# Performance work log

Hardware: AMD Instinct MI355X
Metric: run time of the kernel (lower is better)

Reference implementation:

```python
import jax, jax.numpy as jnp
import numpy as np

B, T, D = 512, 128, 512   # batch, encoder positions, input_size
H = 512                   # hidden_size
MID, BOT = 38, 38         # class counts


def setup_inputs() -> dict:
    key = jax.random.key(0)
    ks = jax.random.split(key, 12)
    s = lambda fan_in: 1.0 / np.sqrt(fan_in)
    inp = {
        "batch_H": jax.random.normal(ks[0], (B, T, D), dtype=jnp.float32),
        "mid_prev_text": jax.random.randint(ks[1], (B, 26), 0, MID, dtype=jnp.int64)
            if jax.config.jax_enable_x64 else jax.random.randint(ks[1], (B, 26), 0, MID).astype(jnp.int32),
        "bot_text": jax.random.randint(ks[2], (B, 26), 0, BOT).astype(jnp.int32),
        # AttentionCell params
        "W_i2h": jax.random.uniform(ks[3], (H, D), jnp.float32, -s(D), s(D)),
        "W_h2h": jax.random.uniform(ks[4], (H, H), jnp.float32, -s(H), s(H)),
        "b_h2h": jax.random.uniform(ks[5], (H,), jnp.float32, -s(H), s(H)),
        "W_score": jax.random.uniform(ks[6], (1, H), jnp.float32, -s(H), s(H)),
        # LSTMCell params: input dim = D + MID + BOT
        "W_ih": jax.random.uniform(ks[7], (4 * H, D + MID + BOT), jnp.float32, -s(H), s(H)),
        "W_hh": jax.random.uniform(ks[8], (4 * H, H), jnp.float32, -s(H), s(H)),
        "b_ih": jax.random.uniform(ks[9], (4 * H,), jnp.float32, -s(H), s(H)),
        "b_hh": jax.random.uniform(ks[10], (4 * H,), jnp.float32, -s(H), s(H)),
        # generator
        "W_gen": jax.random.uniform(ks[11], (MID, H), jnp.float32, -s(H), s(H)),
        "b_gen": jnp.zeros((MID,), jnp.float32),
        "batch_max_length": 25,
    }
    return inp


def reference(batch_H, mid_prev_text, bot_text, W_i2h, W_h2h, b_h2h, W_score,
              W_ih, W_hh, b_ih, b_hh, W_gen, b_gen, batch_max_length):
    num_steps = batch_max_length + 1
    bsz = batch_H.shape[0]
    hid = W_h2h.shape[0]

    # batch_H projection is step-independent: compute once. [B, T, H]
    batch_H_proj = jnp.einsum('btd,hd->bth', batch_H, W_i2h)

    # Precompute teacher-forced onehots, time-major: [num_steps, B, C]
    oh_mid = jax.nn.one_hot(mid_prev_text[:, :num_steps].T, MID, dtype=batch_H.dtype)
    oh_bot = jax.nn.one_hot(bot_text[:, :num_steps].T, BOT, dtype=batch_H.dtype)

    def step(carry, inputs):
        h, c = carry
        ohm, ohb = inputs
        # attention scores over T positions
        prev_proj = h @ W_h2h.T + b_h2h                       # [B, H]
        e = jnp.einsum('bth,oh->bto', jnp.tanh(batch_H_proj + prev_proj[:, None, :]), W_score)  # [B,T,1]
        alpha = jax.nn.softmax(e, axis=1)                     # [B, T, 1]
        context = jnp.einsum('bto,btd->bd', alpha, batch_H)   # [B, D]
        x = jnp.concatenate([context, ohm, ohb], axis=1)      # [B, D+MID+BOT]
        # LSTMCell (PyTorch gate order: i, f, g, o)
        gates = x @ W_ih.T + b_ih + h @ W_hh.T + b_hh         # [B, 4H]
        i_g, f_g, g_g, o_g = jnp.split(gates, 4, axis=1)
        i_g = jax.nn.sigmoid(i_g)
        f_g = jax.nn.sigmoid(f_g)
        g_g = jnp.tanh(g_g)
        o_g = jax.nn.sigmoid(o_g)
        c_new = f_g * c + i_g * g_g
        h_new = o_g * jnp.tanh(c_new)
        return (h_new, c_new), h_new

    h0 = jnp.zeros((bsz, hid), batch_H.dtype)
    c0 = jnp.zeros((bsz, hid), batch_H.dtype)
    (_, _), hiddens = jax.lax.scan(step, (h0, c0), (oh_mid, oh_bot))  # [S, B, H]
    output_hiddens = jnp.transpose(hiddens, (1, 0, 2))                 # [B, S, H]
    g = jnp.einsum('bsh,ch->bsc', output_hiddens, W_gen) + b_gen       # [B, S, MID]
    return g
```

## Files before the change

kernel.cpp:

```cpp
#include <hip/hip_runtime.h>
#include <hip/hip_bf16.h>
#include <hip/hip_fp16.h>
#include <cstdint>
#include <cstddef>

#define B_   512
#define T_   128
#define D_   512
#define H_   512
#define MID_ 38
#define BOT_ 38
#define S_   26
#define XL_  588

typedef unsigned short u16;
typedef __attribute__((ext_vector_type(8))) short bf16x8v;
typedef __attribute__((ext_vector_type(8))) _Float16 f16x8v;
typedef __attribute__((ext_vector_type(8))) unsigned short u16x8;
typedef __attribute__((ext_vector_type(4))) float f32x4v;

__device__ __forceinline__ u16 f2bf_rn(float f){
  unsigned u = __float_as_uint(f);
  return (u16)((u + 0x7fffu + ((u>>16)&1u)) >> 16);
}
__device__ __forceinline__ float bf2f(u16 v){ return __uint_as_float(((unsigned)v)<<16); }
__device__ __forceinline__ u16 f2h_u(float f){ return __half_as_ushort(__float2half(f)); }
__device__ __forceinline__ float h2f_u(u16 u){ return __half2float(__ushort_as_half(u)); }

__device__ __forceinline__ float fast_tanh(float x){
  return 1.0f - 2.0f*__builtin_amdgcn_rcpf(__expf(2.0f*x) + 1.0f);
}
__device__ __forceinline__ float fast_sig(float x){
  return __builtin_amdgcn_rcpf(1.0f + __expf(-x));
}

__device__ __forceinline__ void cvt_hilo4(const float* src, u16* hi, u16* lo){
  float4 v = *(const float4*)src;
  ushort4 h, l;
  h.x=f2bf_rn(v.x); h.y=f2bf_rn(v.y); h.z=f2bf_rn(v.z); h.w=f2bf_rn(v.w);
  l.x=f2bf_rn(v.x-bf2f(h.x)); l.y=f2bf_rn(v.y-bf2f(h.y));
  l.z=f2bf_rn(v.z-bf2f(h.z)); l.w=f2bf_rn(v.w-bf2f(h.w));
  *(ushort4*)hi = h; *(ushort4*)lo = l;
}

__global__ __launch_bounds__(256) void setup_all(
    const float* __restrict__ bH,
    const float* __restrict__ Wi2h, const float* __restrict__ Wh2h,
    const float* __restrict__ Whh,  const float* __restrict__ Wih,
    const float* __restrict__ Wgen, const float* __restrict__ bh2h,
    const float* __restrict__ bih,  const float* __restrict__ bhh,
    u16* __restrict__ bHh,
    u16* __restrict__ Wi2h_h, u16* __restrict__ Bh2_hi, u16* __restrict__ Bh2_lo,
    u16* __restrict__ Bih_hi, u16* __restrict__ Bih_lo,
    u16* __restrict__ Wg_hi,  u16* __restrict__ Wg_lo,
    float* __restrict__ WmT, float* __restrict__ WbT, float* __restrict__ bcombF,
    u16* __restrict__ hA_hi, u16* __restrict__ hA_lo, float* __restrict__ c)
{
  const int T0 = 8388608;
  const int T1 = T0+65536;
  const int T2 = T1+65536;
  const int T3 = T2+262144;
  const int T4 = T3+262144;
  const int T5 = T4+8192;
  const int T6 = T5+19456;
  const int T7 = T6+640;
  const int T8 = T7+65536;
  const int T9 = T8+65536;
  for (int i = blockIdx.x*256 + threadIdx.x; i < T9; i += gridDim.x*256){
    if (i < T0){
      int row=i>>7, c4=(i&127)*4;
      float4 v = *(const float4*)&bH[(size_t)row*512 + c4];
      ushort4 h; h.x=f2h_u(v.x); h.y=f2h_u(v.y); h.z=f2h_u(v.z); h.w=f2h_u(v.w);
      *(ushort4*)&bHh[(size_t)row*512 + c4] = h;
    } else if (i < T1){
      int j=i-T0, row=j>>7, c4=(j&127)*4;
      float4 v = *(const float4*)&Wi2h[(size_t)row*512 + c4];
      ushort4 h; h.x=f2h_u(v.x); h.y=f2h_u(v.y); h.z=f2h_u(v.z); h.w=f2h_u(v.w);
      *(ushort4*)&Wi2h_h[(size_t)row*512 + c4] = h;
    } else if (i < T2){
      int j=i-T1, row=j>>7, c4=(j&127)*4;
      cvt_hilo4(&Wh2h[(size_t)row*512+c4], &Bh2_hi[(size_t)row*512+c4], &Bh2_lo[(size_t)row*512+c4]);
    } else if (i < T3){
      int j=i-T2, row=j>>7, c4=(j&127)*4;
      cvt_hilo4(&Whh[(size_t)row*512+c4],
                &Bh2_hi[(size_t)(512+row)*512+c4], &Bh2_lo[(size_t)(512+row)*512+c4]);
    } else if (i < T4){
      int j=i-T3, row=j>>7, c4=(j&127)*4;
      cvt_hilo4(&Wih[(size_t)row*XL_+c4], &Bih_hi[(size_t)row*512+c4], &Bih_lo[(size_t)row*512+c4]);
    } else if (i < T5){
      int j=i-T4, row=j>>7, c4=(j&127)*4;
      float4 v = make_float4(0.f,0.f,0.f,0.f);
      if (row < MID_) v = *(const float4*)&Wgen[(size_t)row*512 + c4];
      ushort4 h, l;
      h.x=f2bf_rn(v.x); h.y=f2bf_rn(v.y); h.z=f2bf_rn(v.z); h.w=f2bf_rn(v.w);
      l.x=f2bf_rn(v.x-bf2f(h.x)); l.y=f2bf_rn(v.y-bf2f(h.y));
      l.z=f2bf_rn(v.z-bf2f(h.z)); l.w=f2bf_rn(v.w-bf2f(h.w));
      *(ushort4*)&Wg_hi[(size_t)row*512+c4] = h;
      *(ushort4*)&Wg_lo[(size_t)row*512+c4] = l;
    } else if (i < T6){
      int j=i-T5;
      int cc=j>>9, jq=j&511;
#pragma unroll
      for (int u=0;u<4;u++){
        int jj=jq*4+u;
        WmT[(size_t)cc*2048+jj] = Wih[(size_t)jj*XL_ + 512 + cc];
        WbT[(size_t)cc*2048+jj] = Wih[(size_t)jj*XL_ + 512 + MID_ + cc];
      }
    } else if (i < T7){
      int j=(i-T6)*4;
#pragma unroll
      for (int u=0;u<4;u++){
        int k=j+u;
        if (k < 512) bcombF[k] = bh2h[k];
        else if (k < 2560) bcombF[k] = bih[k-512] + bhh[k-512];
      }
    } else if (i < T8){
      int j=i-T7;
      ushort4 z = {0,0,0,0};
      *(ushort4*)&hA_hi[(size_t)j*4] = z;
      *(ushort4*)&hA_lo[(size_t)j*4] = z;
    } else {
      int j=i-T8;
      *(float4*)&c[(size_t)j*4] = make_float4(0.f,0.f,0.f,0.f);
    }
  }
}

__global__ __launch_bounds__(256) void gemm_proj16(
    const u16* __restrict__ Ah, const u16* __restrict__ Bh,
    u16* __restrict__ projh)
{
  extern __shared__ char smem[];
  constexpr int STR = 72;
  short* As = (short*)smem;
  short* Bs = As + 128*STR;
  const int tid=threadIdx.x;
  const int n = blockIdx.x;
  const int x = n & 7, q = n >> 3;
  const int bn = (q & 3) * 128;
  const int bm = ((q >> 2)*8 + x) * 128;
  const int w=tid>>6, lane=tid&63, wr=w>>1, wc=w&1;
  const int srow = tid>>1, shalf = (tid&1)*32;

  f32x4v acc[4][4];
#pragma unroll
  for (int i=0;i<4;i++)
#pragma unroll
    for (int j=0;j<4;j++) acc[i][j] = (f32x4v){0.f,0.f,0.f,0.f};

  u16x8 r0[8], r1[8];
  auto loadTo = [&](u16x8* r, int it){
    const int kk = it<<6;
    const size_t ao = (size_t)(bm+srow)*512 + kk + shalf;
    const size_t bo = (size_t)(bn+srow)*512 + kk + shalf;
#pragma unroll
    for (int qq=0;qq<4;qq++) r[qq]   = *(const u16x8*)&Ah[ao + qq*8];
#pragma unroll
    for (int qq=0;qq<4;qq++) r[4+qq] = *(const u16x8*)&Bh[bo + qq*8];
  };
  auto stage = [&](const u16x8* r){
#pragma unroll
    for (int qq=0;qq<4;qq++) *(u16x8*)&As[srow*STR + shalf + qq*8] = r[qq];
#pragma unroll
    for (int qq=0;qq<4;qq++) *(u16x8*)&Bs[srow*STR + shalf + qq*8] = r[4+qq];
  };
  const int koff = (lane>>4)*8, mrow = lane&15;
  auto compute = [&](){
#pragma unroll
    for (int ks=0;ks<2;ks++)
#pragma unroll
      for (int i=0;i<4;i++)
#pragma unroll
        for (int j=0;j<4;j++){
          f16x8v af = *(const f16x8v*)&As[(wr*64+i*16+mrow)*STR + ks*32 + koff];
          f16x8v bf = *(const f16x8v*)&Bs[(wc*64+j*16+mrow)*STR + ks*32 + koff];
          acc[i][j] = __builtin_amdgcn_mfma_f32_16x16x32_f16(af, bf, acc[i][j], 0,0,0);
        }
  };

  loadTo(r0, 0);
  for (int it=0; it<8; it+=2){
    __syncthreads();
    stage(r0);
    if (it+1 < 8) loadTo(r1, it+1);
    __syncthreads();
    compute();
    if (it+1 >= 8) break;
    __syncthreads();
    stage(r1);
    if (it+2 < 8) loadTo(r0, it+2);
    __syncthreads();
    compute();
  }

  const int r0i = (lane>>4)*4, cn = lane&15;
  __syncthreads();
  u16* Ts = (u16*)smem;
#pragma unroll
  for (int i=0;i<4;i++)
#pragma unroll
    for (int j=0;j<4;j++)
#pragma unroll
      for (int r=0;r<4;r++)
        Ts[(wr*64+i*16+r0i+r)*128 + wc*64+j*16+cn] = f2h_u(acc[i][j][r]);
  __syncthreads();
#pragma unroll
  for (int q2=0;q2<8;q2++){
    int idx = q2*256 + tid;
    int row = idx>>4, c8 = (idx&15)*8;
    *(float4*)&projh[(size_t)(bm+row)*512 + bn + c8] = *(const float4*)&Ts[row*128 + c8];
  }
}

template<int MODE>
__global__ __launch_bounds__(256) void gemm_bf64(
    const u16* __restrict__ Ah, const u16* __restrict__ Al, int lda,
    const u16* __restrict__ Bh, const u16* __restrict__ Bl, int ldb,
    float* __restrict__ Cout, int ldc, const float* __restrict__ bias2)
{
  constexpr int STR = 72;
  __shared__ short Ash[64*STR];
  __shared__ short Asl[64*STR];
  __shared__ short Bsh[64*STR];
  __shared__ short Bsl[64*STR];
  const int tid=threadIdx.x, lane=tid&63, w=tid>>6, wr=w>>1, wc=w&1;
  const int bm=blockIdx.y*64, bn=blockIdx.x*64;
  const int mrow=lane&15, koff=(lane>>4)*8;
  const int srow=tid>>2, scc=(tid&3)*8;

  f32x4v acc[2][2];
#pragma unroll
  for (int i=0;i<2;i++)
#pragma unroll
    for (int j=0;j<2;j++) acc[i][j] = (f32x4v){0.f,0.f,0.f,0.f};

  u16x8 r0[8], r1[8];
  auto loadTo = [&](u16x8* r, int it){
    const int kk = it<<6;
    const size_t ao = (size_t)(bm+srow)*lda + kk + scc;
    const size_t bo = (size_t)(bn+srow)*ldb + kk + scc;
    r[0] = *(const u16x8*)&Ah[ao];   r[1] = *(const u16x8*)&Ah[ao+32];
    r[2] = *(const u16x8*)&Al[ao];   r[3] = *(const u16x8*)&Al[ao+32];
    r[4] = *(const u16x8*)&Bh[bo];   r[5] = *(const u16x8*)&Bh[bo+32];
    r[6] = *(const u16x8*)&Bl[bo];   r[7] = *(const u16x8*)&Bl[bo+32];
  };
  auto stage = [&](const u16x8* r){
    *(u16x8*)&Ash[srow*STR+scc]    = r[0];
    *(u16x8*)&Ash[srow*STR+scc+32] = r[1];
    *(u16x8*)&Asl[srow*STR+scc]    = r[2];
    *(u16x8*)&Asl[srow*STR+scc+32] = r[3];
    *(u16x8*)&Bsh[srow*STR+scc]    = r[4];
    *(u16x8*)&Bsh[srow*STR+scc+32] = r[5];
    *(u16x8*)&Bsl[srow*STR+scc]    = r[6];
    *(u16x8*)&Bsl[srow*STR+scc+32] = r[7];
  };
  auto compute = [&](){
#pragma unroll
    for (int i=0;i<2;i++)
#pragma unroll
      for (int j=0;j<2;j++)
#pragma unroll
        for (int ks=0;ks<2;ks++){
          const int ar = (wr*32+i*16+mrow)*STR + ks*32 + koff;
          const int br = (wc*32+j*16+mrow)*STR + ks*32 + koff;
          bf16x8v ah = *(const bf16x8v*)&Ash[ar];
          bf16x8v al = *(const bf16x8v*)&Asl[ar];
          bf16x8v bh = *(const bf16x8v*)&Bsh[br];
          bf16x8v bl = *(const bf16x8v*)&Bsl[br];
          acc[i][j] = __builtin_amdgcn_mfma_f32_16x16x32_bf16(ah, bh, acc[i][j], 0,0,0);
          acc[i][j] = __builtin_amdgcn_mfma_f32_16x16x32_bf16(ah, bl, acc[i][j], 0,0,0);
          acc[i][j] = __builtin_amdgcn_mfma_f32_16x16x32_bf16(al, bh, acc[i][j], 0,0,0);
        }
  };

  loadTo(r0, 0);
  for (int it=0; it<8; it+=2){
    __syncthreads();
    stage(r0);
    if (it+1 < 8) loadTo(r1, it+1);
    __syncthreads();
    compute();
    if (it+1 >= 8) break;
    __syncthreads();
    stage(r1);
    if (it+2 < 8) loadTo(r0, it+2);
    __syncthreads();
    compute();
  }

  const int r0i = (lane>>4)*4, cn = lane&15;
  if constexpr (MODE==2){
#pragma unroll
    for (int i=0;i<2;i++)
#pragma unroll
      for (int j=0;j<2;j++)
#pragma unroll
        for (int r=0;r<4;r++){
          int m = bm + wr*32 + i*16 + r0i + r;
          int n2 = bn + wc*32 + j*16 + cn;
          if (n2 < MID_){
            int s = m >> 9, b = m & 511;
            Cout[((size_t)b*S_ + s)*MID_ + n2] = acc[i][j][r] + bias2[n2];
          }
        }
  } else {
#pragma unroll
    for (int i=0;i<2;i++)
#pragma unroll
      for (int j=0;j<2;j++)
#pragma unroll
        for (int r=0;r<4;r++){
          int row = bm + wr*32 + i*16 + r0i + r;
          int col = bn + wc*32 + j*16 + cn;
          float v = acc[i][j][r];
          if (bias2) v += bias2[col];
          Cout[(size_t)row*ldc + col] = v;
        }
  }
}

__global__ __launch_bounds__(1024) void attn_kernel(
    const u16* __restrict__ projh, const float* __restrict__ combo,
    const float* __restrict__ Wscore, const u16* __restrict__ bHh,
    u16* __restrict__ ctx_hi, u16* __restrict__ ctx_lo)
{
  __shared__ float s_e[T_];
  __shared__ float s_part[16][D_];
  const int tid=threadIdx.x, b=blockIdx.x, wave=tid>>6, lane=tid&63;

  float pv[8], wv[8];
  {
    const float* pprow = combo + (size_t)b*2560;
    float4 p0=*(const float4*)&pprow[lane*8], p1=*(const float4*)&pprow[lane*8+4];
    float4 w0=*(const float4*)&Wscore[lane*8], w1=*(const float4*)&Wscore[lane*8+4];
    pv[0]=p0.x;pv[1]=p0.y;pv[2]=p0.z;pv[3]=p0.w;pv[4]=p1.x;pv[5]=p1.y;pv[6]=p1.z;pv[7]=p1.w;
    wv[0]=w0.x;wv[1]=w0.y;wv[2]=w0.z;wv[3]=w0.w;wv[4]=w1.x;wv[5]=w1.y;wv[6]=w1.z;wv[7]=w1.w;
  }
  {
    const u16* base = projh + (size_t)b*T_*H_ + lane*8;
    u16x8 rA[4], rB[4];
#pragma unroll
    for (int k=0;k<4;k++) rA[k] = *(const u16x8*)(base + (size_t)(wave+16*k)*H_);
#pragma unroll
    for (int k=0;k<4;k++) rB[k] = *(const u16x8*)(base + (size_t)(wave+16*(k+4))*H_);
#pragma unroll
    for (int k=0;k<4;k++){
      float acc = 0.f;
#pragma unroll
      for (int j=0;j<8;j++) acc += wv[j]*fast_tanh(h2f_u(rA[k][j]) + pv[j]);
#pragma unroll
      for (int o=32;o>0;o>>=1) acc += __shfl_down(acc,o);
      if (lane==0) s_e[wave+16*k] = acc;
    }
#pragma unroll
    for (int k=0;k<4;k++){
      float acc = 0.f;
#pragma unroll
      for (int j=0;j<8;j++) acc += wv[j]*fast_tanh(h2f_u(rB[k][j]) + pv[j]);
#pragma unroll
      for (int o=32;o>0;o>>=1) acc += __shfl_down(acc,o);
      if (lane==0) s_e[wave+16*(k+4)] = acc;
    }
  }
  __syncthreads();
  if (wave==0){
    float p0 = __expf(s_e[lane]), p1 = __expf(s_e[lane+64]);
    float ss = p0 + p1;
#pragma unroll
    for (int o=32;o>0;o>>=1) ss += __shfl_xor(ss,o);
    const float inv = __builtin_amdgcn_rcpf(ss);
    s_e[lane]    = p0*inv;
    s_e[lane+64] = p1*inv;
  }
  __syncthreads();

  const int d0 = lane*8;
  float a[8] = {0,0,0,0,0,0,0,0};
  {
    const u16* base = bHh + (size_t)b*T_*D_ + d0;
    const int t0 = wave*8;
    u16x8 rr[8];
#pragma unroll
    for (int r=0;r<8;r++) rr[r] = *(const u16x8*)(base + (size_t)(t0+r)*D_);
#pragma unroll
    for (int r=0;r<8;r++){
      const float al = s_e[t0+r];
#pragma unroll
      for (int j=0;j<8;j++) a[j] += al*h2f_u(rr[r][j]);
    }
  }
  *(float4*)&s_part[wave][d0]   = make_float4(a[0],a[1],a[2],a[3]);
  *(float4*)&s_part[wave][d0+4] = make_float4(a[4],a[5],a[6],a[7]);
  __syncthreads();
  if (tid < D_){
    float vv = s_part[0][tid];
#pragma unroll
    for (int q=1;q<16;q++) vv += s_part[q][tid];
    u16 hh=f2bf_rn(vv), ll=f2bf_rn(vv-bf2f(hh));
    ctx_hi[(size_t)b*512 + tid] = hh;
    ctx_lo[(size_t)b*512 + tid] = ll;
  }
}

__global__ __launch_bounds__(256) void gates_lstm(
    const u16* __restrict__ Ah, const u16* __restrict__ Al,
    const u16* __restrict__ Bh, const u16* __restrict__ Bl,
    const float* __restrict__ combo,
    const float* __restrict__ WmT, const float* __restrict__ WbT,
    const int* __restrict__ midtok, const int* __restrict__ bottok,
    float* __restrict__ c,
    u16* __restrict__ hA_hi, u16* __restrict__ hA_lo,
    u16* __restrict__ hid_hi, u16* __restrict__ hid_lo, int s)
{
  constexpr int STR = 72;
  __shared__ short Bsh[64*STR];
  __shared__ short Bsl[64*STR];
  const int tid=threadIdx.x, lane=tid&63, w=tid>>6;
  const int j0 = blockIdx.x*16, bm = blockIdx.y*64;
  const int mrow=lane&15, koff=(lane>>4)*8;
  const int arow = bm + w*16 + mrow;
  const int srow = tid>>2, scc=(tid&3)*8;
  const int sbrow = (srow>>4)*512 + j0 + (srow&15);

  f32x4v acc[4];
#pragma unroll
  for (int f=0;f<4;f++) acc[f] = (f32x4v){0.f,0.f,0.f,0.f};

  u16x8 rb0[4], rb1[4];
  bf16x8v a0[4], a1[4];
  auto loadB = [&](u16x8* r, int it){
    const int kk = it<<6;
    const size_t bo = (size_t)sbrow*512 + kk + scc;
    r[0] = *(const u16x8*)&Bh[bo];   r[1] = *(const u16x8*)&Bh[bo+32];
    r[2] = *(const u16x8*)&Bl[bo];   r[3] = *(const u16x8*)&Bl[bo+32];
  };
  auto loadA = [&](bf16x8v* a, int it){
    const int kk = it<<6;
    const size_t ao = (size_t)arow*512 + kk + koff;
    a[0] = *(const bf16x8v*)&Ah[ao];  a[1] = *(const bf16x8v*)&Ah[ao+32];
    a[2] = *(const bf16x8v*)&Al[ao];  a[3] = *(const bf16x8v*)&Al[ao+32];
  };
  auto stage = [&](const u16x8* r){
    *(u16x8*)&Bsh[srow*STR+scc]    = r[0];
    *(u16x8*)&Bsh[srow*STR+scc+32] = r[1];
    *(u16x8*)&Bsl[srow*STR+scc]    = r[2];
    *(u16x8*)&Bsl[srow*STR+scc+32] = r[3];
  };
  auto compute = [&](const bf16x8v* a){
#pragma unroll
    for (int f=0;f<4;f++)
#pragma unroll
      for (int ks=0;ks<2;ks++){
        const int br = (f*16+mrow)*STR + ks*32 + koff;
        bf16x8v bh = *(const bf16x8v*)&Bsh[br];
        bf16x8v bl = *(const bf16x8v*)&Bsl[br];
        acc[f] = __builtin_amdgcn_mfma_f32_16x16x32_bf16(a[ks],   bh, acc[f], 0,0,0);
        acc[f] = __builtin_amdgcn_mfma_f32_16x16x32_bf16(a[ks],   bl, acc[f], 0,0,0);
        acc[f] = __builtin_amdgcn_mfma_f32_16x16x32_bf16(a[ks+2], bh, acc[f], 0,0,0);
      }
  };

  loadB(rb0, 0); loadA(a0, 0);
  for (int it=0; it<8; it+=2){
    __syncthreads();
    stage(rb0);
    if (it+1 < 8){ loadB(rb1, it+1); loadA(a1, it+1); }
    __syncthreads();
    compute(a0);
    if (it+1 >= 8) break;
    __syncthreads();
    stage(rb1);
    if (it+2 < 8){ loadB(rb0, it+2); loadA(a0, it+2); }
    __syncthreads();
    compute(a1);
  }

  const int r0=(lane>>4)*4, jj=lane&15, j=j0+jj;
#pragma unroll
  for (int r=0;r<4;r++){
    const int b = bm + w*16 + r0 + r;
    const int mt = midtok[b*26 + s];
    const int bt = bottok[b*26 + s];
    const float* wm = WmT + (size_t)mt*2048;
    const float* wb = WbT + (size_t)bt*2048;
    const float* cb = combo + (size_t)b*2560 + 512;
    float ig = acc[0][r] + cb[j       ] + wm[j       ] + wb[j       ];
    float fg = acc[1][r] + cb[512 + j ] + wm[512 + j ] + wb[512 + j ];
    float gg = acc[2][r] + cb[1024 + j] + wm[1024 + j] + wb[1024 + j];
    float og = acc[3][r] + cb[1536 + j] + wm[1536 + j] + wb[1536 + j];
    ig = fast_sig(ig);
    fg = fast_sig(fg);
    gg = fast_tanh(gg);
    og = fast_sig(og);
    const size_t ci = (size_t)b*512 + j;
    const float cn = fg*c[ci] + ig*gg;
    const float hn = og*fast_tanh(cn);
    c[ci] = cn;
    u16 hh = f2bf_rn(hn), hl = f2bf_rn(hn - bf2f(hh));
    hA_hi[ci] = hh;
    hA_lo[ci] = hl;
    hid_hi[((size_t)s*512 + b)*512 + j] = hh;
    hid_lo[((size_t)s*512 + b)*512 + j] = hl;
  }
}

extern "C" void kernel_launch(void* const* d_in, const int* in_sizes, int n_in,
                              void* d_out, int out_size, void* d_ws, size_t ws_size,
                              hipStream_t stream) {
  const float* bH   = (const float*)d_in[0];
  const int*   midt = (const int*)  d_in[1];
  const int*   bott = (const int*)  d_in[2];
  const float* Wi2h = (const float*)d_in[3];
  const float* Wh2h = (const float*)d_in[4];
  const float* bh2h = (const float*)d_in[5];
  const float* Wsc  = (const float*)d_in[6];
  const float* Wih  = (const float*)d_in[7];
  const float* Whh  = (const float*)d_in[8];
  const float* bih  = (const float*)d_in[9];
  const float* bhh  = (const float*)d_in[10];
  const float* Wgen = (const float*)d_in[11];
  const float* bgen = (const float*)d_in[12];
  float* out = (float*)d_out;

  char* wp = (char*)d_ws;
  u16* projh   = (u16*)wp; wp += (size_t)B_*T_*H_*2;
  u16* bHh     = (u16*)wp; wp += (size_t)B_*T_*D_*2;
  u16* Bh2_hi  = (u16*)wp; wp += (size_t)2560*512*2;
  u16* Bh2_lo  = (u16*)wp; wp += (size_t)2560*512*2;
  u16* Bih_hi  = (u16*)wp; wp += (size_t)2048*512*2;
  u16* Bih_lo  = (u16*)wp; wp += (size_t)2048*512*2;
  u16* Wi2h_h  = (u16*)wp; wp += (size_t)512*512*2;
  u16* Wg_hi   = (u16*)wp; wp += (size_t)64*512*2;
  u16* Wg_lo   = (u16*)wp; wp += (size_t)64*512*2;
  u16* ctx_hi  = (u16*)wp; wp += (size_t)B_*512*2;
  u16* ctx_lo  = (u16*)wp; wp += (size_t)B_*512*2;
  u16* hA_hi   = (u16*)wp; wp += (size_t)B_*512*2;
  u16* hA_lo   = (u16*)wp; wp += (size_t)B_*512*2;
  u16* hid_hi  = (u16*)wp; wp += (size_t)S_*B_*H_*2;
  u16* hid_lo  = (u16*)wp; wp += (size_t)S_*B_*H_*2;
  float* combo = (float*)wp; wp += (size_t)B_*2560*4;
  float* c     = (float*)wp; wp += (size_t)B_*H_*4;
  float* bcombF= (float*)wp; wp += (size_t)2560*4;
  float* WmT   = (float*)wp; wp += (size_t)MID_*2048*4;
  float* WbT   = (float*)wp; wp += (size_t)BOT_*2048*4;
  if ((size_t)(wp - (char*)d_ws) > ws_size) return;

  setup_all<<<4096, 256, 0, stream>>>(
      bH, Wi2h, Wh2h, Whh, Wih, Wgen, bh2h, bih, bhh,
      bHh, Wi2h_h, Bh2_hi, Bh2_lo, Bih_hi, Bih_lo, Wg_hi, Wg_lo,
      WmT, WbT, bcombF, hA_hi, hA_lo, c);

  gemm_proj16<<<2048, 256, 36864, stream>>>(bHh, Wi2h_h, projh);

  for (int s=0; s<S_; ++s){
    gemm_bf64<0><<<dim3(40,8), 256, 0, stream>>>(
        hA_hi, hA_lo, 512, Bh2_hi, Bh2_lo, 512,
        combo, 2560, bcombF);
    attn_kernel<<<B_, 1024, 0, stream>>>(
        projh, combo, Wsc, bHh, ctx_hi, ctx_lo);
    gates_lstm<<<dim3(32,8), 256, 0, stream>>>(
        ctx_hi, ctx_lo, Bih_hi, Bih_lo, combo, WmT, WbT,
        midt, bott, c, hA_hi, hA_lo,
        hid_hi, hid_lo, s);
  }

  gemm_bf64<2><<<dim3(1,208), 256, 0, stream>>>(
      hid_hi, hid_lo, 512, Wg_hi, Wg_lo, 512,
      out, 0, bgen);
}
```

Measured before the change: 1.328 ms.

## Fuse attention scoring, softmax and context accumulation into single pass

The attention kernel now has each wave handle 16 time positions end to end. Each wave computes the score, exponentiates it without max subtraction, and accumulates the unnormalized context and the denominator in registers, with normalization applied once at the end. This removes two block-wide barriers and the separate softmax pass, and halves block size to 512 threads. It relies on scores staying small enough that exp without max-shift does not overflow, and it uses full xor reductions per score.

```diff
diff --git a/kernel.cpp b/kernel.cpp
--- a/kernel.cpp
+++ b/kernel.cpp
@@ -319,14 +319,15 @@
   }
 }
 
-__global__ __launch_bounds__(1024) void attn_kernel(
+__global__ __launch_bounds__(512) void attn_kernel(
     const u16* __restrict__ projh, const float* __restrict__ combo,
     const float* __restrict__ Wscore, const u16* __restrict__ bHh,
     u16* __restrict__ ctx_hi, u16* __restrict__ ctx_lo)
 {
-  __shared__ float s_e[T_];
-  __shared__ float s_part[16][D_];
+  __shared__ float s_part[8][D_];
+  __shared__ float s_den[8];
   const int tid=threadIdx.x, b=blockIdx.x, wave=tid>>6, lane=tid&63;
+  const int d0 = lane*8;
 
   float pv[8], wv[8];
   {
@@ -336,66 +337,49 @@
     pv[0]=p0.x;pv[1]=p0.y;pv[2]=p0.z;pv[3]=p0.w;pv[4]=p1.x;pv[5]=p1.y;pv[6]=p1.z;pv[7]=p1.w;
     wv[0]=w0.x;wv[1]=w0.y;wv[2]=w0.z;wv[3]=w0.w;wv[4]=w1.x;wv[5]=w1.y;wv[6]=w1.z;wv[7]=w1.w;
   }
-  {
-    const u16* base = projh + (size_t)b*T_*H_ + lane*8;
-    u16x8 rA[4], rB[4];
-#pragma unroll
-    for (int k=0;k<4;k++) rA[k] = *(const u16x8*)(base + (size_t)(wave+16*k)*H_);
-#pragma unroll
-    for (int k=0;k<4;k++) rB[k] = *(const u16x8*)(base + (size_t)(wave+16*(k+4))*H_);
-#pragma unroll
-    for (int k=0;k<4;k++){
-      float acc = 0.f;
-#pragma unroll
-      for (int j=0;j<8;j++) acc += wv[j]*fast_tanh(h2f_u(rA[k][j]) + pv[j]);
-#pragma unroll
-      for (int o=32;o>0;o>>=1) acc += __shfl_down(acc,o);
-      if (lane==0) s_e[wave+16*k] = acc;
+
+  const u16* pbase = projh + (size_t)b*T_*H_ + lane*8;
+  const u16* cbase = bHh  + (size_t)b*T_*D_ + d0;
+  const int t0 = wave*16;
+
+  float a[8] = {0,0,0,0,0,0,0,0};
+  float den = 0.f;
+
+#pragma unroll
+  for (int bt=0; bt<4; ++bt){
+    const int tb = t0 + bt*4;
+    u16x8 rp[4], rc[4];
+#pragma unroll
+    for (int r=0;r<4;r++) rp[r] = *(const u16x8*)(pbase + (size_t)(tb+r)*H_);
+#pragma unroll
+    for (int r=0;r<4;r++) rc[r] = *(const u16x8*)(cbase + (size_t)(tb+r)*D_);
+#pragma unroll
+    for (int r=0;r<4;r++){
+      float e = 0.f;
+#pragma unroll
+      for (int j=0;j<8;j++) e += wv[j]*fast_tanh(h2f_u(rp[r][j]) + pv[j]);
+#pragma unroll
+      for (int o=32;o>0;o>>=1) e += __shfl_xor(e,o);
+      const float p = __expf(e);
+      den += p;
+#pragma unroll
+      for (int j=0;j<8;j++) a[j] += p*h2f_u(rc[r][j]);
     }
-#pragma unroll
-    for (int k=0;k<4;k++){
-      float acc = 0.f;
-#pragma unroll
-      for (int j=0;j<8;j++) acc += wv[j]*fast_tanh(h2f_u(rB[k][j]) + pv[j]);
-#pragma unroll
-      for (int o=32;o>0;o>>=1) acc += __shfl_down(acc,o);
-      if (lane==0) s_e[wave+16*(k+4)] = acc;
-    }
-  }
-  __syncthreads();
-  if (wave==0){
-    float p0 = __expf(s_e[lane]), p1 = __expf(s_e[lane+64]);
-    float ss = p0 + p1;
-#pragma unroll
-    for (int o=32;o>0;o>>=1) ss += __shfl_xor(ss,o);
-    const float inv = __builtin_amdgcn_rcpf(ss);
-    s_e[lane]    = p0*inv;
-    s_e[lane+64] = p1*inv;
-  }
-  __syncthreads();
-
-  const int d0 = lane*8;
-  float a[8] = {0,0,0,0,0,0,0,0};
-  {
-    const u16* base = bHh + (size_t)b*T_*D_ + d0;
-    const int t0 = wave*8;
-    u16x8 rr[8];
-#pragma unroll
-    for (int r=0;r<8;r++) rr[r] = *(const u16x8*)(base + (size_t)(t0+r)*D_);
-#pragma unroll
-    for (int r=0;r<8;r++){
-      const float al = s_e[t0+r];
-#pragma unroll
-      for (int j=0;j<8;j++) a[j] += al*h2f_u(rr[r][j]);
-    }
-  }
+  }
+
   *(float4*)&s_part[wave][d0]   = make_float4(a[0],a[1],a[2],a[3]);
   *(float4*)&s_part[wave][d0+4] = make_float4(a[4],a[5],a[6],a[7]);
+  if (lane==0) s_den[wave] = den;
   __syncthreads();
-  if (tid < D_){
+
+  {
     float vv = s_part[0][tid];
 #pragma unroll
-    for (int q=1;q<16;q++) vv += s_part[q][tid];
+    for (int q=1;q<8;q++) vv += s_part[q][tid];
+    float dd = s_den[0];
+#pragma unroll
+    for (int q=1;q<8;q++) dd += s_den[q];
+    vv *= __builtin_amdgcn_rcpf(dd);
     u16 hh=f2bf_rn(vv), ll=f2bf_rn(vv-bf2f(hh));
     ctx_hi[(size_t)b*512 + tid] = hh;
     ctx_lo[(size_t)b*512 + tid] = ll;
@@ -556,7 +540,7 @@
     gemm_bf64<0><<<dim3(40,8), 256, 0, stream>>>(
         hA_hi, hA_lo, 512, Bh2_hi, Bh2_lo, 512,
         combo, 2560, bcombF);
-    attn_kernel<<<B_, 1024, 0, stream>>>(
+    attn_kernel<<<B_, 512, 0, stream>>>(
         projh, combo, Wsc, bHh, ctx_hi, ctx_lo);
     gates_lstm<<<dim3(32,8), 256, 0, stream>>>(
         ctx_hi, ctx_lo, Bih_hi, Bih_lo, combo, WmT, WbT,
```

Result: slower. 1.472 ms (+10.9%).
